# Kernel tuning notes

Hardware: AMD Instinct MI355X
Metric: run time of the kernel (lower is better)

Reference implementation:

```python
import jax, jax.numpy as jnp
import numpy as np

B, D, E, H, T = 16384, 32, 8, 64, 10  # batch, state_dim, n_experts, hidden, time points
TEMP = 1.0  # gating temperature


def setup_inputs() -> dict:
    key = jax.random.key(0)
    ks = jax.random.split(key, 12)
    w = lambda k, shape, fan_in: (jax.random.normal(k, shape, jnp.float32) / np.sqrt(fan_in)).astype(jnp.float32)
    return {
        "x0": jax.random.normal(ks[0], (B, D), jnp.float32),
        "t_span": jnp.linspace(0.0, 1.0, T).astype(jnp.float32),
        # per-expert time-conditioned MLP: (x, t) -> H -> H -> D
        "W1": w(ks[1], (E, D + 1, H), D + 1), "b1": jnp.zeros((E, H), jnp.float32),
        "W2": w(ks[2], (E, H, H), H),          "b2": jnp.zeros((E, H), jnp.float32),
        "W3": w(ks[3], (E, H, D), H),          "b3": jnp.zeros((E, D), jnp.float32),
        # gating MLP on concat(x, dx_init): 2D -> H -> E
        "Gw1": w(ks[4], (2 * D, H), 2 * D), "Gb1": jnp.zeros((H,), jnp.float32),
        "Gw2": w(ks[5], (H, E), H),         "Gb2": jnp.zeros((E,), jnp.float32),
    }


def _dyn(t, x, W1, b1, W2, b2, W3, b3, Gw1, Gb1, Gw2, Gb2):
    # AME-ODE training-path dynamics: uniform-weighted init, gate, weighted sum
    inp = jnp.concatenate([x, jnp.ones((x.shape[0], 1), x.dtype) * t], axis=-1)  # [B, D+1]
    h = jnp.tanh(jnp.einsum('bi,eih->beh', inp, W1) + b1)
    h = jnp.tanh(jnp.einsum('beh,ehg->beg', h, W2) + b2)
    f = jnp.einsum('beg,egd->bed', h, W3) + b3          # all-expert dynamics [B, E, D]
    dx_init = f.mean(axis=1)                             # uniform weights 1/E
    g = jnp.tanh(jnp.concatenate([x, dx_init], -1) @ Gw1 + Gb1)
    wgt = jax.nn.softmax((g @ Gw2 + Gb2) / TEMP, axis=-1)  # [B, E]
    return jnp.einsum('be,bed->bd', wgt, f)


def reference(x0, t_span, W1, b1, W2, b2, W3, b3, Gw1, Gb1, Gw2, Gb2):
    params = (W1, b1, W2, b2, W3, b3, Gw1, Gb1, Gw2, Gb2)

    def step(x, ts):
        t0, t1 = ts[0], ts[1]
        dt = t1 - t0
        k1 = _dyn(t0, x, *params)
        k2 = _dyn(t0 + 0.5 * dt, x + 0.5 * dt * k1, *params)
        k3 = _dyn(t0 + 0.5 * dt, x + 0.5 * dt * k2, *params)
        k4 = _dyn(t1, x + dt * k3, *params)
        xn = x + (dt / 6.0) * (k1 + 2.0 * k2 + 2.0 * k3 + k4)
        return xn, xn

    pairs = jnp.stack([t_span[:-1], t_span[1:]], axis=1)  # [T-1, 2]
    _, traj = jax.lax.scan(step, x0, pairs)               # [T-1, B, D]
    traj = jnp.concatenate([x0[None], traj], axis=0)       # [T, B, D]
    return jnp.transpose(traj, (1, 0, 2))                  # [B, T, D]
```

## Files before the change

### kernel.cpp

```cpp
#include <hip/hip_runtime.h>
#include <hip/hip_bf16.h>

typedef unsigned int u32;
typedef unsigned short u16;
typedef __attribute__((ext_vector_type(8))) short short8;
typedef __attribute__((ext_vector_type(4))) float f32x4;
typedef __attribute__((ext_vector_type(4))) u32 u32x4;
typedef __attribute__((ext_vector_type(2))) u32 u32x2;

#define DD 32
#define EE 8
#define HH 64
#define TT 10
#define BATCH 16384
#define EPB 64

__device__ __forceinline__ float fast_tanh(float x) {
  float e = __expf(2.f * x);
  return 1.f - 2.f * __builtin_amdgcn_rcpf(e + 1.f);
}
__device__ __forceinline__ u16 f2b_rn(float v) {
  return (u16)((__float_as_uint(v) + 0x8000u) >> 16);
}
__device__ __forceinline__ u32 pack2_rn(float a, float b) {
  return __builtin_amdgcn_perm(__float_as_uint(b) + 0x8000u,
                               __float_as_uint(a) + 0x8000u, 0x07060302u);
}
__device__ __forceinline__ float unp_lo(u32 p) { return __uint_as_float(p << 16); }
__device__ __forceinline__ float unp_hi(u32 p) { return __uint_as_float(p & 0xffff0000u); }
__device__ __forceinline__ short8 lds_frag(const u32* p) {
  u32x4 w = *(const u32x4*)p;
  return __builtin_bit_cast(short8, w);
}
__device__ __forceinline__ f32x4 bcast4(float v) { f32x4 c; c[0]=v; c[1]=v; c[2]=v; c[3]=v; return c; }

__global__ __launch_bounds__(512) void ame_ode_kernel(
    const float* __restrict__ x0, const float* __restrict__ tspan,
    const float* __restrict__ W1, const float* __restrict__ b1,
    const float* __restrict__ W2, const float* __restrict__ b2,
    const float* __restrict__ W3, const float* __restrict__ b3,
    const float* __restrict__ Gw1, const float* __restrict__ Gb1,
    const float* __restrict__ Gw2, const float* __restrict__ Gb2,
    float* __restrict__ out)
{
  __shared__ __align__(16) u32 xdb[EPB][36];
  __shared__ __align__(16) u32 fs[EPB][130];
  __shared__ __align__(16) float lg[EPB][12];
  __shared__ __align__(16) u32 hsbuf[EE * 16 * 36];

  const int tid  = threadIdx.x;
  const int lane = tid & 63;
  const int l15  = lane & 15;
  const int quad = lane >> 4;
  const int e    = __builtin_amdgcn_readfirstlane(tid >> 6);
  const int b    = blockIdx.x * EPB + lane;

  const float* W1f = W1 + e * (DD + 1) * HH;
  const float* b1f = b1 + e * HH;
  const float* W2f = W2 + e * HH * HH;
  const float* b2f = b2 + e * HH;
  const float* W3f = W3 + e * HH * DD;
  const float* b3f = b3 + e * DD;

  short8 bw1[4], bw2[2][4], bw3[2][2];
  #pragma unroll
  for (int nt = 0; nt < 4; nt++)
    #pragma unroll
    for (int j = 0; j < 8; j++)
      bw1[nt][j] = (short)f2b_rn(W1f[(quad * 8 + j) * HH + nt * 16 + l15]);
  #pragma unroll
  for (int ks = 0; ks < 2; ks++)
    #pragma unroll
    for (int nt = 0; nt < 4; nt++)
      #pragma unroll
      for (int j = 0; j < 8; j++)
        bw2[ks][nt][j] = (short)f2b_rn(W2f[(ks * 32 + quad * 8 + j) * HH + nt * 16 + l15]);
  #pragma unroll
  for (int ks = 0; ks < 2; ks++)
    #pragma unroll
    for (int dt2 = 0; dt2 < 2; dt2++)
      #pragma unroll
      for (int j = 0; j < 8; j++)
        bw3[ks][dt2][j] = (short)f2b_rn(W3f[(ks * 32 + quad * 8 + j) * DD + dt2 * 16 + l15]);

  const int g1mt = e & 3;
  const int g1n0 = (e >> 2) * 2;
  short8 bg1[2][2];
  #pragma unroll
  for (int ni = 0; ni < 2; ni++)
    #pragma unroll
    for (int ks = 0; ks < 2; ks++)
      #pragma unroll
      for (int j = 0; j < 8; j++)
        bg1[ni][ks][j] = (short)f2b_rn(Gw1[(ks * 32 + quad * 8 + j) * HH + (g1n0 + ni) * 16 + l15]);
  const float gb1a = Gb1[g1n0 * 16 + l15];
  const float gb1b = Gb1[(g1n0 + 1) * 16 + l15];

  short8 bg2[2];
  float gb2v = 0.f;
  if (e < 4) {
    #pragma unroll
    for (int ks = 0; ks < 2; ks++)
      #pragma unroll
      for (int j = 0; j < 8; j++)
        bg2[ks][j] = (short)((l15 < 8) ? f2b_rn(Gw2[(ks * 32 + quad * 8 + j) * EE + l15]) : 0);
    gb2v = (l15 < 8) ? Gb2[l15] : 0.f;
  }

  u32 c1p[4];
  #pragma unroll
  for (int nt = 0; nt < 4; nt++)
    c1p[nt] = pack2_rn(b1f[nt * 16 + l15], W1f[DD * HH + nt * 16 + l15]);
  f32x4 c2i[4], c3i[2];
  #pragma unroll
  for (int nt = 0; nt < 4; nt++) c2i[nt] = bcast4(b2f[nt * 16 + l15]);
  #pragma unroll
  for (int dt2 = 0; dt2 < 2; dt2++) c3i[dt2] = bcast4(b3f[dt2 * 16 + l15]);

  float xst[4], xacc[4];
  {
    const float4 v = *(const float4*)(x0 + b * DD + 4 * e);
    xst[0] = v.x; xst[1] = v.y; xst[2] = v.z; xst[3] = v.w;
    xacc[0] = v.x; xacc[1] = v.y; xacc[2] = v.z; xacc[3] = v.w;
    u32x2 p; p.x = pack2_rn(v.x, v.y); p.y = pack2_rn(v.z, v.w);
    *(u32x2*)&xdb[lane][2 * e] = p;
    *(float4*)(out + b * TT * DD + 4 * e) = v;
  }
  __syncthreads();

  u32* const hw   = hsbuf + e * 576;
  u16* const hw16 = (u16*)hw;
  u16* const fw16 = (u16*)&fs[0][0];
  u16* const uw16 = (u16*)hsbuf;
  const u32* const u32v = hsbuf;

  #pragma unroll 1
  for (int step = 0; step < TT - 1; step++) {
    const float t0 = tspan[step];
    const float t1 = tspan[step + 1];
    const float dt = t1 - t0;

    #pragma unroll 1
    for (int s = 0; s < 4; s++) {
      const float tcur = (s == 0) ? t0 : ((s == 3) ? t1 : t0 + 0.5f * dt);

      f32x4 c1i[4];
      #pragma unroll
      for (int nt = 0; nt < 4; nt++)
        c1i[nt] = bcast4(__builtin_fmaf(tcur, unp_hi(c1p[nt]), unp_lo(c1p[nt])));

      #pragma unroll 2
      for (int mt = 0; mt < 4; mt++) {
        const short8 a1 = lds_frag(&xdb[mt * 16 + l15][quad * 4]);
        f32x4 h1a[4];
        #pragma unroll
        for (int nt = 0; nt < 4; nt++)
          h1a[nt] = __builtin_amdgcn_mfma_f32_16x16x32_bf16(a1, bw1[nt], c1i[nt], 0, 0, 0);
        #pragma unroll
        for (int nt = 0; nt < 4; nt++)
          #pragma unroll
          for (int r = 0; r < 4; r++)
            hw16[(quad * 4 + r) * 72 + nt * 16 + l15] = f2b_rn(fast_tanh(h1a[nt][r]));

        f32x4 h2a[4];
        #pragma unroll
        for (int nt = 0; nt < 4; nt++) h2a[nt] = c2i[nt];
        #pragma unroll
        for (int ks = 0; ks < 2; ks++) {
          const short8 a2 = lds_frag(&hw[l15 * 36 + ks * 16 + quad * 4]);
          #pragma unroll
          for (int nt = 0; nt < 4; nt++)
            h2a[nt] = __builtin_amdgcn_mfma_f32_16x16x32_bf16(a2, bw2[ks][nt], h2a[nt], 0, 0, 0);
        }
        #pragma unroll
        for (int nt = 0; nt < 4; nt++)
          #pragma unroll
          for (int r = 0; r < 4; r++)
            hw16[(quad * 4 + r) * 72 + nt * 16 + l15] = f2b_rn(fast_tanh(h2a[nt][r]));

        f32x4 fa[2];
        #pragma unroll
        for (int dt2 = 0; dt2 < 2; dt2++) fa[dt2] = c3i[dt2];
        #pragma unroll
        for (int ks = 0; ks < 2; ks++) {
          const short8 a3 = lds_frag(&hw[l15 * 36 + ks * 16 + quad * 4]);
          #pragma unroll
          for (int dt2 = 0; dt2 < 2; dt2++)
            fa[dt2] = __builtin_amdgcn_mfma_f32_16x16x32_bf16(a3, bw3[ks][dt2], fa[dt2], 0, 0, 0);
        }
        #pragma unroll
        for (int dt2 = 0; dt2 < 2; dt2++)
          #pragma unroll
          for (int r = 0; r < 4; r++)
            fw16[(mt * 16 + quad * 4 + r) * 260 + e * 32 + dt2 * 16 + l15] = f2b_rn(fa[dt2][r]);
      }
      __syncthreads();

      {
        float s0 = 0.f, s1 = 0.f, s2 = 0.f, s3 = 0.f;
        #pragma unroll
        for (int j = 0; j < EE; j++) {
          const u32x2 p = *(const u32x2*)&fs[lane][j * 16 + 2 * e];
          s0 += unp_lo(p.x); s1 += unp_hi(p.x);
          s2 += unp_lo(p.y); s3 += unp_hi(p.y);
        }
        u32x2 w; w.x = pack2_rn(s0 * 0.125f, s1 * 0.125f);
        w.y = pack2_rn(s2 * 0.125f, s3 * 0.125f);
        *(u32x2*)&xdb[lane][16 + 2 * e] = w;
      }
      __syncthreads();

      {
        f32x4 u0 = bcast4(gb1a), u1 = bcast4(gb1b);
        #pragma unroll
        for (int ks = 0; ks < 2; ks++) {
          const short8 ag = lds_frag(&xdb[g1mt * 16 + l15][ks * 16 + quad * 4]);
          u0 = __builtin_amdgcn_mfma_f32_16x16x32_bf16(ag, bg1[0][ks], u0, 0, 0, 0);
          u1 = __builtin_amdgcn_mfma_f32_16x16x32_bf16(ag, bg1[1][ks], u1, 0, 0, 0);
        }
        #pragma unroll
        for (int r = 0; r < 4; r++) {
          uw16[(g1mt * 16 + quad * 4 + r) * 72 + g1n0 * 16 + l15]       = f2b_rn(fast_tanh(u0[r]));
          uw16[(g1mt * 16 + quad * 4 + r) * 72 + (g1n0 + 1) * 16 + l15] = f2b_rn(fast_tanh(u1[r]));
        }
      }
      __syncthreads();

      if (e < 4) {
        f32x4 lv = bcast4(gb2v);
        #pragma unroll
        for (int ks = 0; ks < 2; ks++) {
          const short8 ag = lds_frag(&u32v[(e * 16 + l15) * 36 + ks * 16 + quad * 4]);
          lv = __builtin_amdgcn_mfma_f32_16x16x32_bf16(ag, bg2[ks], lv, 0, 0, 0);
        }
        if (l15 < 8) {
          #pragma unroll
          for (int r = 0; r < 4; r++)
            lg[e * 16 + quad * 4 + r][l15] = lv[r];
        }
      }
      __syncthreads();

      {
        const float4 la0 = *(const float4*)&lg[lane][0];
        const float4 la1 = *(const float4*)&lg[lane][4];
        float m = fmaxf(fmaxf(fmaxf(la0.x, la0.y), fmaxf(la0.z, la0.w)),
                        fmaxf(fmaxf(la1.x, la1.y), fmaxf(la1.z, la1.w)));
        float w8[EE];
        w8[0] = __expf(la0.x - m); w8[1] = __expf(la0.y - m);
        w8[2] = __expf(la0.z - m); w8[3] = __expf(la0.w - m);
        w8[4] = __expf(la1.x - m); w8[5] = __expf(la1.y - m);
        w8[6] = __expf(la1.z - m); w8[7] = __expf(la1.w - m);
        float ss = 0.f;
        #pragma unroll
        for (int j = 0; j < EE; j++) ss += w8[j];
        const float inv = __builtin_amdgcn_rcpf(ss);

        float kc[4] = {0.f, 0.f, 0.f, 0.f};
        #pragma unroll
        for (int j = 0; j < EE; j++) {
          const float wg = w8[j] * inv;
          const u32x2 p = *(const u32x2*)&fs[lane][j * 16 + 2 * e];
          kc[0] = __builtin_fmaf(wg, unp_lo(p.x), kc[0]);
          kc[1] = __builtin_fmaf(wg, unp_hi(p.x), kc[1]);
          kc[2] = __builtin_fmaf(wg, unp_lo(p.y), kc[2]);
          kc[3] = __builtin_fmaf(wg, unp_hi(p.y), kc[3]);
        }

        const float wk = (s == 1 || s == 2) ? 2.f : 1.f;
        const float ak = dt * (1.f / 6.f) * wk;
        #pragma unroll
        for (int q = 0; q < 4; q++) xacc[q] = __builtin_fmaf(ak, kc[q], xacc[q]);

        float xn[4];
        if (s < 3) {
          const float cn = (s == 2) ? dt : 0.5f * dt;
          #pragma unroll
          for (int q = 0; q < 4; q++) xn[q] = __builtin_fmaf(cn, kc[q], xst[q]);
        } else {
          #pragma unroll
          for (int q = 0; q < 4; q++) { xst[q] = xacc[q]; xn[q] = xacc[q]; }
          float4 o; o.x = xn[0]; o.y = xn[1]; o.z = xn[2]; o.w = xn[3];
          *(float4*)(out + (b * TT + step + 1) * DD + 4 * e) = o;
        }
        u32x2 p; p.x = pack2_rn(xn[0], xn[1]); p.y = pack2_rn(xn[2], xn[3]);
        *(u32x2*)&xdb[lane][2 * e] = p;
      }
      __syncthreads();
    }
  }
}

extern "C" void kernel_launch(void* const* d_in, const int* in_sizes, int n_in,
                              void* d_out, int out_size, void* d_ws, size_t ws_size,
                              hipStream_t stream)
{
  const float* x0    = (const float*)d_in[0];
  const float* tspan = (const float*)d_in[1];
  const float* W1  = (const float*)d_in[2];
  const float* b1  = (const float*)d_in[3];
  const float* W2  = (const float*)d_in[4];
  const float* b2  = (const float*)d_in[5];
  const float* W3  = (const float*)d_in[6];
  const float* b3  = (const float*)d_in[7];
  const float* Gw1 = (const float*)d_in[8];
  const float* Gb1 = (const float*)d_in[9];
  const float* Gw2 = (const float*)d_in[10];
  const float* Gb2 = (const float*)d_in[11];

  ame_ode_kernel<<<BATCH / EPB, 512, 0, stream>>>(
      x0, tspan, W1, b1, W2, b2, W3, b3, Gw1, Gb1, Gw2, Gb2, (float*)d_out);
}
```

Measured before the change: 328.9 us.

## Fold expert-mean into gating GEMM and drop a barrier stage

Instead of computing the uniform mean of expert outputs separately and writing it into the x buffer, the gating first layer now multiplies the full expert output buffer by Gw1's dx half pre-scaled by 1/8. The mean is folded into the weights, which removes one LDS pass and one __syncthreads per RK stage at the cost of more MFMAs. The bias vectors are also packed to bf16 pairs to cut register pressure, which lowers their precision. tanh now uses exp2 with a folded constant.

Result: no change. 329.6 us (+0.2%).

```diff
diff --git a/kernel.cpp b/kernel.cpp
--- a/kernel.cpp
+++ b/kernel.cpp
@@ -15,8 +15,14 @@
 #define BATCH 16384
 #define EPB 64
 
+#if __has_builtin(__builtin_amdgcn_exp2f)
+#define EXP2F(x) __builtin_amdgcn_exp2f(x)
+#else
+#define EXP2F(x) __builtin_exp2f(x)
+#endif
+
 __device__ __forceinline__ float fast_tanh(float x) {
-  float e = __expf(2.f * x);
+  float e = EXP2F(x * 2.885390082f);
   return 1.f - 2.f * __builtin_amdgcn_rcpf(e + 1.f);
 }
 __device__ __forceinline__ u16 f2b_rn(float v) {
@@ -29,8 +35,8 @@
 __device__ __forceinline__ float unp_lo(u32 p) { return __uint_as_float(p << 16); }
 __device__ __forceinline__ float unp_hi(u32 p) { return __uint_as_float(p & 0xffff0000u); }
 __device__ __forceinline__ short8 lds_frag(const u32* p) {
-  u32x4 w = *(const u32x4*)p;
-  return __builtin_bit_cast(short8, w);
+  u32x4 v = *(const u32x4*)p;
+  return __builtin_bit_cast(short8, v);
 }
 __device__ __forceinline__ f32x4 bcast4(float v) { f32x4 c; c[0]=v; c[1]=v; c[2]=v; c[3]=v; return c; }
 
@@ -43,10 +49,10 @@
     const float* __restrict__ Gw2, const float* __restrict__ Gb2,
     float* __restrict__ out)
 {
-  __shared__ __align__(16) u32 xdb[EPB][36];
-  __shared__ __align__(16) u32 fs[EPB][130];
-  __shared__ __align__(16) float lg[EPB][12];
-  __shared__ __align__(16) u32 hsbuf[EE * 16 * 36];
+  __shared__ __align__(16) u32  xdb[EPB * 20];
+  __shared__ __align__(16) u32  fsb[EPB * 132];
+  __shared__ __align__(16) float lg[EPB * 12];
+  __shared__ __align__(16) u32  hsbuf[EE * 16 * 36];
 
   const int tid  = threadIdx.x;
   const int lane = tid & 63;
@@ -85,14 +91,14 @@
 
   const int g1mt = e & 3;
   const int g1n0 = (e >> 2) * 2;
-  short8 bg1[2][2];
+  short8 bg1x[2], bg1f[2];
   #pragma unroll
   for (int ni = 0; ni < 2; ni++)
     #pragma unroll
-    for (int ks = 0; ks < 2; ks++)
-      #pragma unroll
-      for (int j = 0; j < 8; j++)
-        bg1[ni][ks][j] = (short)f2b_rn(Gw1[(ks * 32 + quad * 8 + j) * HH + (g1n0 + ni) * 16 + l15]);
+    for (int j = 0; j < 8; j++) {
+      bg1x[ni][j] = (short)f2b_rn(Gw1[(quad * 8 + j) * HH + (g1n0 + ni) * 16 + l15]);
+      bg1f[ni][j] = (short)f2b_rn(0.125f * Gw1[(DD + quad * 8 + j) * HH + (g1n0 + ni) * 16 + l15]);
+    }
   const float gb1a = Gb1[g1n0 * 16 + l15];
   const float gb1b = Gb1[(g1n0 + 1) * 16 + l15];
 
@@ -107,15 +113,14 @@
     gb2v = (l15 < 8) ? Gb2[l15] : 0.f;
   }
 
-  u32 c1p[4];
+  u32 c1p[4], c2p[2], c3p;
   #pragma unroll
   for (int nt = 0; nt < 4; nt++)
     c1p[nt] = pack2_rn(b1f[nt * 16 + l15], W1f[DD * HH + nt * 16 + l15]);
-  f32x4 c2i[4], c3i[2];
-  #pragma unroll
-  for (int nt = 0; nt < 4; nt++) c2i[nt] = bcast4(b2f[nt * 16 + l15]);
-  #pragma unroll
-  for (int dt2 = 0; dt2 < 2; dt2++) c3i[dt2] = bcast4(b3f[dt2 * 16 + l15]);
+  #pragma unroll
+  for (int p = 0; p < 2; p++)
+    c2p[p] = pack2_rn(b2f[(2 * p) * 16 + l15], b2f[(2 * p + 1) * 16 + l15]);
+  c3p = pack2_rn(b3f[l15], b3f[16 + l15]);
 
   float xst[4], xacc[4];
   {
@@ -123,16 +128,14 @@
     xst[0] = v.x; xst[1] = v.y; xst[2] = v.z; xst[3] = v.w;
     xacc[0] = v.x; xacc[1] = v.y; xacc[2] = v.z; xacc[3] = v.w;
     u32x2 p; p.x = pack2_rn(v.x, v.y); p.y = pack2_rn(v.z, v.w);
-    *(u32x2*)&xdb[lane][2 * e] = p;
+    *(u32x2*)&xdb[lane * 20 + 2 * e] = p;
     *(float4*)(out + b * TT * DD + 4 * e) = v;
   }
   __syncthreads();
 
   u32* const hw   = hsbuf + e * 576;
   u16* const hw16 = (u16*)hw;
-  u16* const fw16 = (u16*)&fs[0][0];
-  u16* const uw16 = (u16*)hsbuf;
-  const u32* const u32v = hsbuf;
+  u16* const fw16 = (u16*)fsb;
 
   #pragma unroll 1
   for (int step = 0; step < TT - 1; step++) {
@@ -151,7 +154,7 @@
 
       #pragma unroll 2
       for (int mt = 0; mt < 4; mt++) {
-        const short8 a1 = lds_frag(&xdb[mt * 16 + l15][quad * 4]);
+        const short8 a1 = lds_frag(&xdb[(mt * 16 + l15) * 20 + quad * 4]);
         f32x4 h1a[4];
         #pragma unroll
         for (int nt = 0; nt < 4; nt++)
@@ -164,7 +167,8 @@
 
         f32x4 h2a[4];
         #pragma unroll
-        for (int nt = 0; nt < 4; nt++) h2a[nt] = c2i[nt];
+        for (int nt = 0; nt < 4; nt++)
+          h2a[nt] = bcast4((nt & 1) ? unp_hi(c2p[nt >> 1]) : unp_lo(c2p[nt >> 1]));
         #pragma unroll
         for (int ks = 0; ks < 2; ks++) {
           const short8 a2 = lds_frag(&hw[l15 * 36 + ks * 16 + quad * 4]);
@@ -180,7 +184,8 @@
 
         f32x4 fa[2];
         #pragma unroll
-        for (int dt2 = 0; dt2 < 2; dt2++) fa[dt2] = c3i[dt2];
+        for (int dt2 = 0; dt2 < 2; dt2++)
+          fa[dt2] = bcast4(dt2 ? unp_hi(c3p) : unp_lo(c3p));
         #pragma unroll
         for (int ks = 0; ks < 2; ks++) {
           const short8 a3 = lds_frag(&hw[l15 * 36 + ks * 16 + quad * 4]);
@@ -192,58 +197,49 @@
         for (int dt2 = 0; dt2 < 2; dt2++)
           #pragma unroll
           for (int r = 0; r < 4; r++)
-            fw16[(mt * 16 + quad * 4 + r) * 260 + e * 32 + dt2 * 16 + l15] = f2b_rn(fa[dt2][r]);
+            fw16[(mt * 16 + quad * 4 + r) * 264 + e * 32 + dt2 * 16 + l15] = f2b_rn(fa[dt2][r]);
       }
       __syncthreads();
 
       {
-        float s0 = 0.f, s1 = 0.f, s2 = 0.f, s3 = 0.f;
-        #pragma unroll
-        for (int j = 0; j < EE; j++) {
-          const u32x2 p = *(const u32x2*)&fs[lane][j * 16 + 2 * e];
-          s0 += unp_lo(p.x); s1 += unp_hi(p.x);
-          s2 += unp_lo(p.y); s3 += unp_hi(p.y);
-        }
-        u32x2 w; w.x = pack2_rn(s0 * 0.125f, s1 * 0.125f);
-        w.y = pack2_rn(s2 * 0.125f, s3 * 0.125f);
-        *(u32x2*)&xdb[lane][16 + 2 * e] = w;
+        f32x4 u0 = bcast4(gb1a), u1 = bcast4(gb1b);
+        const int mg = g1mt * 16 + l15;
+        const short8 ax = lds_frag(&xdb[mg * 20 + quad * 4]);
+        u0 = __builtin_amdgcn_mfma_f32_16x16x32_bf16(ax, bg1x[0], u0, 0, 0, 0);
+        u1 = __builtin_amdgcn_mfma_f32_16x16x32_bf16(ax, bg1x[1], u1, 0, 0, 0);
+        #pragma unroll
+        for (int kb = 0; kb < 8; kb++) {
+          const short8 af = lds_frag(&fsb[mg * 132 + kb * 16 + quad * 4]);
+          u0 = __builtin_amdgcn_mfma_f32_16x16x32_bf16(af, bg1f[0], u0, 0, 0, 0);
+          u1 = __builtin_amdgcn_mfma_f32_16x16x32_bf16(af, bg1f[1], u1, 0, 0, 0);
+        }
+        u16* const us16 = (u16*)hsbuf;
+        #pragma unroll
+        for (int r = 0; r < 4; r++) {
+          us16[(g1mt * 16 + quad * 4 + r) * 72 + g1n0 * 16 + l15]       = f2b_rn(fast_tanh(u0[r]));
+          us16[(g1mt * 16 + quad * 4 + r) * 72 + (g1n0 + 1) * 16 + l15] = f2b_rn(fast_tanh(u1[r]));
+        }
       }
       __syncthreads();
 
-      {
-        f32x4 u0 = bcast4(gb1a), u1 = bcast4(gb1b);
+      if (e < 4) {
+        f32x4 lv = bcast4(gb2v);
         #pragma unroll
         for (int ks = 0; ks < 2; ks++) {
-          const short8 ag = lds_frag(&xdb[g1mt * 16 + l15][ks * 16 + quad * 4]);
-          u0 = __builtin_amdgcn_mfma_f32_16x16x32_bf16(ag, bg1[0][ks], u0, 0, 0, 0);
-          u1 = __builtin_amdgcn_mfma_f32_16x16x32_bf16(ag, bg1[1][ks], u1, 0, 0, 0);
-        }
-        #pragma unroll
-        for (int r = 0; r < 4; r++) {
-          uw16[(g1mt * 16 + quad * 4 + r) * 72 + g1n0 * 16 + l15]       = f2b_rn(fast_tanh(u0[r]));
-          uw16[(g1mt * 16 + quad * 4 + r) * 72 + (g1n0 + 1) * 16 + l15] = f2b_rn(fast_tanh(u1[r]));
+          const short8 ag = lds_frag(&hsbuf[(e * 16 + l15) * 36 + ks * 16 + quad * 4]);
+          lv = __builtin_amdgcn_mfma_f32_16x16x32_bf16(ag, bg2[ks], lv, 0, 0, 0);
+        }
+        if (l15 < 8) {
+          #pragma unroll
+          for (int r = 0; r < 4; r++)
+            lg[(e * 16 + quad * 4 + r) * 12 + l15] = lv[r];
         }
       }
       __syncthreads();
 
-      if (e < 4) {
-        f32x4 lv = bcast4(gb2v);
-        #pragma unroll
-        for (int ks = 0; ks < 2; ks++) {
-          const short8 ag = lds_frag(&u32v[(e * 16 + l15) * 36 + ks * 16 + quad * 4]);
-          lv = __builtin_amdgcn_mfma_f32_16x16x32_bf16(ag, bg2[ks], lv, 0, 0, 0);
-        }
-        if (l15 < 8) {
-          #pragma unroll
-          for (int r = 0; r < 4; r++)
-            lg[e * 16 + quad * 4 + r][l15] = lv[r];
-        }
-      }
-      __syncthreads();
-
       {
-        const float4 la0 = *(const float4*)&lg[lane][0];
-        const float4 la1 = *(const float4*)&lg[lane][4];
+        const float4 la0 = *(const float4*)&lg[lane * 12 + 0];
+        const float4 la1 = *(const float4*)&lg[lane * 12 + 4];
         float m = fmaxf(fmaxf(fmaxf(la0.x, la0.y), fmaxf(la0.z, la0.w)),
                         fmaxf(fmaxf(la1.x, la1.y), fmaxf(la1.z, la1.w)));
         float w8[EE];
@@ -260,7 +256,7 @@
         #pragma unroll
         for (int j = 0; j < EE; j++) {
           const float wg = w8[j] * inv;
-          const u32x2 p = *(const u32x2*)&fs[lane][j * 16 + 2 * e];
+          const u32x2 p = *(const u32x2*)&fsb[lane * 132 + j * 16 + 2 * e];
           kc[0] = __builtin_fmaf(wg, unp_lo(p.x), kc[0]);
           kc[1] = __builtin_fmaf(wg, unp_hi(p.x), kc[1]);
           kc[2] = __builtin_fmaf(wg, unp_lo(p.y), kc[2]);
@@ -284,7 +280,7 @@
           *(float4*)(out + (b * TT + step + 1) * DD + 4 * e) = o;
         }
         u32x2 p; p.x = pack2_rn(xn[0], xn[1]); p.y = pack2_rn(xn[2], xn[3]);
-        *(u32x2*)&xdb[lane][2 * e] = p;
+        *(u32x2*)&xdb[lane * 20 + 2 * e] = p;
       }
       __syncthreads();
     }
```
